# Kernel tuning notes

Measured on AMD Instinct MI355X. Metric: run time of the kernel, lower is better.

The kernel has to match this reference:

```python
import jax, jax.numpy as jnp
import numpy as np

N_NODES = 100000

def _gcn_conv(x, W, b, src, dst, deg_inv_sqrt):
    # h = X W  (dense GEMM)
    h = x @ W
    # symmetric normalization: norm_e = d^{-1/2}[src] * d^{-1/2}[dst]
    norm = deg_inv_sqrt[src] * deg_inv_sqrt[dst]
    # gather-scale-scatter aggregation
    msgs = h[src] * norm[:, None]
    out = jax.ops.segment_sum(msgs, dst, num_segments=N_NODES)
    return out + b

def _prep_graph(edge_index):
    # add self loops (PyG GCNConv default)
    loop = jnp.arange(N_NODES, dtype=edge_index.dtype)
    src = jnp.concatenate([edge_index[0], loop])
    dst = jnp.concatenate([edge_index[1], loop])
    deg = jax.ops.segment_sum(jnp.ones_like(dst, dtype=jnp.float32), dst,
                              num_segments=N_NODES)
    deg_inv_sqrt = jnp.where(deg > 0, jax.lax.rsqrt(deg), 0.0)
    return src, dst, deg_inv_sqrt

def setup_inputs() -> dict:
    key = jax.random.key(0)
    ks = jax.random.split(key, 5)
    d_in, d_h, d_out, E = 128, 256, 128, 1600000
    x = jax.random.normal(ks[0], (N_NODES, d_in), dtype=jnp.float32)
    edge_index = jax.random.randint(ks[1], (2, E), 0, N_NODES, dtype=jnp.int64)
    W1 = jax.random.normal(ks[2], (d_in, d_h), dtype=jnp.float32) / np.sqrt(d_in)
    W2 = jax.random.normal(ks[3], (d_h, d_h), dtype=jnp.float32) / np.sqrt(d_h)
    W3 = jax.random.normal(ks[4], (d_h, d_out), dtype=jnp.float32) / np.sqrt(d_h)
    return {"x": x, "edge_index": edge_index,
            "W1": W1, "b1": jnp.zeros((d_h,), jnp.float32),
            "W2": W2, "b2": jnp.zeros((d_h,), jnp.float32),
            "W3": W3, "b3": jnp.zeros((d_out,), jnp.float32)}

def reference(x, edge_index, W1, b1, W2, b2, W3, b3):
    src, dst, dis = _prep_graph(edge_index)
    h = _gcn_conv(x, W1, b1, src, dst, dis)
    h = jax.nn.relu(h)  # dropout is identity in eval mode
    h = _gcn_conv(h, W2, b2, src, dst, dis)
    h = jax.nn.relu(h)
    out = _gcn_conv(h, W3, b3, src, dst, dis)
    return out
```

## Files before the change

### kernel.cpp

```cpp
#include <hip/hip_runtime.h>
#include <hip/hip_bf16.h>

#define N_NODES 100000
#define M_PAD   100096
#define SCAN_B  98

typedef __attribute__((ext_vector_type(8))) short s8v;
typedef __attribute__((ext_vector_type(4))) float f4v;
typedef unsigned short u16;
typedef unsigned int   u32;

__device__ __forceinline__ u16 f2bf(float v) {
    __hip_bfloat16 b = __float2bfloat16(v);
    return __builtin_bit_cast(u16, b);
}
__device__ __forceinline__ float bf2f(u16 u) {
    u32 t = (u32)u << 16;
    return __builtin_bit_cast(float, t);
}
__device__ __forceinline__ float bflo(u32 p) { return __builtin_bit_cast(float, p << 16); }
__device__ __forceinline__ float bfhi(u32 p) { return __builtin_bit_cast(float, p & 0xffff0000u); }

__device__ __forceinline__ void gl_lds16(const void* g, void* l) {
    __builtin_amdgcn_global_load_lds(
        (const __attribute__((address_space(1))) void*)g,
        (__attribute__((address_space(3))) void*)l, 16, 0, 0);
}


__global__ __launch_bounds__(256) void k_zero_int(int* __restrict__ p, int n) {
    int i = blockIdx.x * 256 + threadIdx.x;
    if (i < n) p[i] = 0;
}

__global__ __launch_bounds__(256) void k_count(const int* __restrict__ ei, int E,
                                               int* __restrict__ cnt) {
    const int h = E >> 1;
    for (int i = blockIdx.x * 256 + threadIdx.x; i < h; i += gridDim.x * 256) {
        const int2 d2 = *reinterpret_cast<const int2*>(ei + E + 2 * i);
        atomicAdd(&cnt[d2.x], 1);
        atomicAdd(&cnt[d2.y], 1);
    }
    if (blockIdx.x == 0 && threadIdx.x == 0 && (E & 1))
        atomicAdd(&cnt[ei[E + E - 1]], 1);
}

__global__ __launch_bounds__(1024) void k_scan_a(const int* __restrict__ cnt,
                                                 int* __restrict__ row_ptr,
                                                 int* __restrict__ bsum,
                                                 float* __restrict__ dis, int n) {
    __shared__ int wsum[16];
    const int tid = threadIdx.x;
    const int lane = tid & 63;
    const int wv = tid >> 6;
    const int i = blockIdx.x * 1024 + tid;
    const int v = (i < n) ? cnt[i] : 0;
    if (i < n) dis[i] = 1.0f / sqrtf((float)(v + 1));
    int x = v;
    #pragma unroll
    for (int d = 1; d < 64; d <<= 1) {
        int t = __shfl_up(x, d, 64);
        if (lane >= d) x += t;
    }
    if (lane == 63) wsum[wv] = x;
    __syncthreads();
    int woff = 0, total = 0;
    #pragma unroll
    for (int w = 0; w < 16; ++w) {
        int s = wsum[w];
        if (w < wv) woff += s;
        total += s;
    }
    if (i < n) row_ptr[i] = woff + x - v;
    if (tid == 0) bsum[blockIdx.x] = total;
}

__global__ __launch_bounds__(128) void k_scan_b(int* __restrict__ bsum,
                                                int* __restrict__ row_ptr,
                                                int nparts, int n, int total_edges) {
    __shared__ int w0tot;
    const int tid = threadIdx.x;
    const int lane = tid & 63;
    const int v = (tid < nparts) ? bsum[tid] : 0;
    int x = v;
    #pragma unroll
    for (int d = 1; d < 64; d <<= 1) {
        int t = __shfl_up(x, d, 64);
        if (lane >= d) x += t;
    }
    if (tid == 63) w0tot = x;
    __syncthreads();
    int excl = x - v + ((tid >= 64) ? w0tot : 0);
    if (tid < nparts) bsum[tid] = excl;
    if (tid == 0) row_ptr[n] = total_edges;
}

__global__ __launch_bounds__(1024) void k_scan_c(int* __restrict__ row_ptr,
                                                 const int* __restrict__ bsum,
                                                 int* __restrict__ cursor, int n) {
    const int i = blockIdx.x * 1024 + threadIdx.x;
    if (i < n) {
        const int r = row_ptr[i] + bsum[blockIdx.x];
        row_ptr[i] = r;
        cursor[i] = r;
    }
}

__global__ __launch_bounds__(256) void k_scatter(const int* __restrict__ ei, int E,
                                                 const float* __restrict__ dis,
                                                 int* __restrict__ cursor,
                                                 int2* __restrict__ edat) {
    const int h = E >> 1;
    for (int i = blockIdx.x * 256 + threadIdx.x; i < h; i += gridDim.x * 256) {
        const int2 s2 = *reinterpret_cast<const int2*>(ei + 2 * i);
        const int2 d2 = *reinterpret_cast<const int2*>(ei + E + 2 * i);
        const int p0 = atomicAdd(&cursor[d2.x], 1);
        edat[p0] = make_int2(s2.x, __float_as_int(dis[s2.x] * dis[d2.x]));
        const int p1 = atomicAdd(&cursor[d2.y], 1);
        edat[p1] = make_int2(s2.y, __float_as_int(dis[s2.y] * dis[d2.y]));
    }
    if (blockIdx.x == 0 && threadIdx.x == 0 && (E & 1)) {
        const int e = E - 1;
        const int s = ei[e], d = ei[E + e];
        const int pos = atomicAdd(&cursor[d], 1);
        edat[pos] = make_int2(s, __float_as_int(dis[s] * dis[d]));
    }
}

__global__ __launch_bounds__(256) void k_prep_w_all(
    const float* __restrict__ W1, const float* __restrict__ W2,
    const float* __restrict__ W3,
    u16* __restrict__ w1h, u16* __restrict__ w1l,
    u16* __restrict__ w2h, u16* __restrict__ w2l,
    u16* __restrict__ w3h, u16* __restrict__ w3l) {
    const int b = blockIdx.x;
    const float* W; u16 *H, *L; int K, N, n;
    if (b < 256)      { W = W1; H = w1h; L = w1l; K = 128; N = 256; n = b; }
    else if (b < 512) { W = W2; H = w2h; L = w2l; K = 256; N = 256; n = b - 256; }
    else              { W = W3; H = w3h; L = w3l; K = 256; N = 128; n = b - 512; }
    for (int k = threadIdx.x; k < K; k += 256) {
        float v = W[(size_t)k * N + n];
        u16 hi = f2bf(v);
        H[(size_t)n * K + k] = hi;
        L[(size_t)n * K + k] = f2bf(v - bf2f(hi));
    }
}

__global__ __launch_bounds__(256) void k_x2bf(const float* __restrict__ x,
                                              u16* __restrict__ xb, long n8) {
    long i = (long)blockIdx.x * 256 + threadIdx.x;
    if (i >= n8) return;
    const float4 a = *reinterpret_cast<const float4*>(x + i * 8);
    const float4 b = *reinterpret_cast<const float4*>(x + i * 8 + 4);
    uint4 p;
    p.x = (u32)f2bf(a.x) | ((u32)f2bf(a.y) << 16);
    p.y = (u32)f2bf(a.z) | ((u32)f2bf(a.w) << 16);
    p.z = (u32)f2bf(b.x) | ((u32)f2bf(b.y) << 16);
    p.w = (u32)f2bf(b.z) | ((u32)f2bf(b.w) << 16);
    *reinterpret_cast<uint4*>(xb + i * 8) = p;
}

template <bool BIAS, bool RELU>
__global__ __launch_bounds__(512, 4) void k_gemm2p(
    const u16* __restrict__ A,
    const u16* __restrict__ Bth, const u16* __restrict__ Btl,
    const float* __restrict__ bias,
    u16* __restrict__ Ch,
    int M, int N, int K) {
    __shared__ u16 As[256 * 32];
    __shared__ u16 Bhs[128 * 32];
    __shared__ u16 Bls[128 * 32];

    const int tid  = threadIdx.x;
    const int wid  = tid >> 6;
    const int lane = tid & 63;
    const int wm = wid >> 1;
    const int wn = wid & 1;
    const int row0 = blockIdx.y * 256;
    const int n0   = blockIdx.x * 128;

    const int srow  = lane >> 2;
    const int sbyte = (lane & 3) * 16;
    const int fr = lane & 15;
    const int kg = (lane >> 4) * 8;

    f4v acc[4][4];
    #pragma unroll
    for (int t = 0; t < 4; ++t)
        #pragma unroll
        for (int u = 0; u < 4; ++u)
            acc[t][u] = (f4v){0.f, 0.f, 0.f, 0.f};

    for (int k0 = 0; k0 < K; k0 += 32) {
        #pragma unroll
        for (int g = 0; g < 2; ++g) {
            const int rloc = wid * 32 + g * 16;
            const size_t ga = (size_t)(row0 + rloc + srow) * K + k0;
            gl_lds16((const char*)(A + ga) + sbyte, &As[rloc * 32]);
        }
        {
            const int rloc = wid * 16;
            const size_t gb = (size_t)(n0 + rloc + srow) * K + k0;
            gl_lds16((const char*)(Bth + gb) + sbyte, &Bhs[rloc * 32]);
            gl_lds16((const char*)(Btl + gb) + sbyte, &Bls[rloc * 32]);
        }
        __syncthreads();

        s8v nh[4], nl[4];
        #pragma unroll
        for (int u = 0; u < 4; ++u) {
            const int rb = (wn * 64 + u * 16 + fr) * 32 + kg;
            nh[u] = *(const s8v*)&Bhs[rb];
            nl[u] = *(const s8v*)&Bls[rb];
        }
        #pragma unroll
        for (int t = 0; t < 4; ++t) {
            const int ra = (wm * 64 + t * 16 + fr) * 32 + kg;
            const s8v m = *(const s8v*)&As[ra];
            #pragma unroll
            for (int u = 0; u < 4; ++u) {
                acc[t][u] = __builtin_amdgcn_mfma_f32_16x16x32_bf16(nh[u], m, acc[t][u], 0, 0, 0);
                acc[t][u] = __builtin_amdgcn_mfma_f32_16x16x32_bf16(nl[u], m, acc[t][u], 0, 0, 0);
            }
        }
        __syncthreads();
    }

    const int ncol = (lane >> 4) * 4;
    #pragma unroll
    for (int t = 0; t < 4; ++t) {
        const int grow = row0 + wm * 64 + t * 16 + fr;
        if (grow < M) {
            #pragma unroll
            for (int u = 0; u < 4; ++u) {
                const int nb = n0 + wn * 64 + u * 16 + ncol;
                float v[4];
                #pragma unroll
                for (int r = 0; r < 4; ++r) {
                    float z = acc[t][u][r];
                    if constexpr (BIAS) z += bias[nb + r];
                    if constexpr (RELU) z = fmaxf(z, 0.f);
                    v[r] = z;
                }
                const size_t off = (size_t)grow * N + nb;
                u16 hi[4];
                #pragma unroll
                for (int r = 0; r < 4; ++r) hi[r] = f2bf(v[r]);
                uint2 ph;
                ph.x = (u32)hi[0] | ((u32)hi[1] << 16);
                ph.y = (u32)hi[2] | ((u32)hi[3] << 16);
                *reinterpret_cast<uint2*>(Ch + off) = ph;
            }
        }
    }
}

template <int D, bool BIAS, bool RELU, int OUT_MODE>
__global__ __launch_bounds__(256) void k_agg(
    const u16* __restrict__ h, const int* __restrict__ row_ptr,
    const int2* __restrict__ edat,
    const float* __restrict__ dis, const float* __restrict__ bias,
    float* __restrict__ outf, u16* __restrict__ outh) {
    constexpr int V = D / 64;
    const int wave = threadIdx.x >> 6;
    const int lane = threadIdx.x & 63;
    const int node = blockIdx.x * 4 + wave;
    if (node >= N_NODES) return;

    const int beg = row_ptr[node];
    const int end = row_ptr[node + 1];
    const int base = lane * V;

    float a[4][V];
    #pragma unroll
    for (int c = 0; c < 4; ++c)
        #pragma unroll
        for (int j = 0; j < V; ++j) a[c][j] = 0.f;

#define LOADV(dst, s) do {                                                    \
        const u16* p_ = h + (size_t)(s) * D + base;                           \
        if constexpr (V == 4) {                                               \
            uint2 t_ = *reinterpret_cast<const uint2*>(p_);                   \
            dst[0] = bflo(t_.x); dst[1] = bfhi(t_.x);                         \
            dst[2] = bflo(t_.y); dst[3] = bfhi(t_.y);                         \
        } else {                                                              \
            u32 t_ = *reinterpret_cast<const u32*>(p_);                       \
            dst[0] = bflo(t_); dst[1] = bfhi(t_);                             \
        }                                                                     \
    } while (0)

    int e = beg;
    for (; e + 8 <= end; e += 8) {
        int2 ed[8];
        float v[8][V];
        #pragma unroll
        for (int j = 0; j < 8; ++j) ed[j] = edat[e + j];
        #pragma unroll
        for (int j = 0; j < 8; ++j) LOADV(v[j], ed[j].x);
        #pragma unroll
        for (int j = 0; j < 8; ++j) {
            const float w = __int_as_float(ed[j].y);
            #pragma unroll
            for (int k = 0; k < V; ++k) a[j & 3][k] += v[j][k] * w;
        }
    }
    for (; e + 2 <= end; e += 2) {
        const int2 e0 = edat[e], e1 = edat[e + 1];
        float v0[V], v1[V];
        LOADV(v0, e0.x); LOADV(v1, e1.x);
        const float w0 = __int_as_float(e0.y), w1 = __int_as_float(e1.y);
        #pragma unroll
        for (int k = 0; k < V; ++k) { a[0][k] += v0[k] * w0; a[1][k] += v1[k] * w1; }
    }
    if (e < end) {
        const int2 e0 = edat[e];
        float v0[V];
        LOADV(v0, e0.x);
        const float w0 = __int_as_float(e0.y);
        #pragma unroll
        for (int k = 0; k < V; ++k) a[2][k] += v0[k] * w0;
    }

    {
        float sw = dis[node];
        sw *= sw;
        float vs[V];
        LOADV(vs, node);
        #pragma unroll
        for (int k = 0; k < V; ++k) a[3][k] += vs[k] * sw;
    }
#undef LOADV

    float r[V];
    #pragma unroll
    for (int j = 0; j < V; ++j) {
        float v = (a[0][j] + a[1][j]) + (a[2][j] + a[3][j]);
        if constexpr (BIAS) v += bias[base + j];
        if constexpr (RELU) v = fmaxf(v, 0.f);
        r[j] = v;
    }

    const size_t off = (size_t)node * D + base;
    if constexpr (OUT_MODE == 1) {
        u16 hi[V];
        #pragma unroll
        for (int j = 0; j < V; ++j) hi[j] = f2bf(r[j]);
        if constexpr (V == 4) {
            uint2 ph;
            ph.x = (u32)hi[0] | ((u32)hi[1] << 16);
            ph.y = (u32)hi[2] | ((u32)hi[3] << 16);
            *reinterpret_cast<uint2*>(outh + off) = ph;
        } else {
            *reinterpret_cast<u32*>(outh + off) = (u32)hi[0] | ((u32)hi[1] << 16);
        }
    } else {
        if constexpr (V == 4) {
            *reinterpret_cast<float4*>(outf + off) = make_float4(r[0], r[1], r[2], r[3]);
        } else {
            *reinterpret_cast<float2*>(outf + off) = make_float2(r[0], r[1]);
        }
    }
}


extern "C" void kernel_launch(void* const* d_in, const int* in_sizes, int n_in,
                              void* d_out, int out_size, void* d_ws, size_t ws_size,
                              hipStream_t stream) {
    const float* x  = (const float*)d_in[0];
    const int*   ei = (const int*)d_in[1];
    const float* W1 = (const float*)d_in[2];
    const float* b1 = (const float*)d_in[3];
    const float* W2 = (const float*)d_in[4];
    const float* b2 = (const float*)d_in[5];
    const float* W3 = (const float*)d_in[6];
    const float* b3 = (const float*)d_in[7];
    float* out = (float*)d_out;

    const int N = N_NODES;
    const int E = in_sizes[1] / 2;

    char* ws = (char*)d_ws;
    size_t o = 0;
    auto take = [&](size_t bytes) {
        void* p = ws + o;
        o += (bytes + 255) & ~(size_t)255;
        return p;
    };
    float* dis     = (float*)take((size_t)N * 4);
    int*   row_ptr = (int*)  take((size_t)(N + 1) * 4);
    int*   cnt_cur = (int*)  take((size_t)N * 4);
    int*   bsum    = (int*)  take((size_t)SCAN_B * 4);
    int2*  edat    = (int2*) take((size_t)E * 8);
    u16* wt1h = (u16*)take((size_t)256 * 128 * 2);
    u16* wt1l = (u16*)take((size_t)256 * 128 * 2);
    u16* wt2h = (u16*)take((size_t)256 * 256 * 2);
    u16* wt2l = (u16*)take((size_t)256 * 256 * 2);
    u16* wt3h = (u16*)take((size_t)128 * 256 * 2);
    u16* wt3l = (u16*)take((size_t)128 * 256 * 2);
    char* slot1 = (char*)take((size_t)M_PAD * 256 * 2);
    char* slot2 = (char*)take((size_t)M_PAD * 256 * 2);
    (void)ws_size; (void)n_in; (void)out_size;

    u16* xb = (u16*)slot1;
    u16* h1 = (u16*)slot1;
    u16* h2 = (u16*)slot1;
    u16* xa = (u16*)slot2;
    u16* g2 = (u16*)slot2;
    u16* g3 = (u16*)slot2;

    const int nb_nodes = (N + 255) / 256;
    const int nb_pairs = ((E / 2) + 255) / 256;

    k_zero_int<<<nb_nodes, 256, 0, stream>>>(cnt_cur, N);
    k_count<<<nb_pairs, 256, 0, stream>>>(ei, E, cnt_cur);
    k_scan_a<<<SCAN_B, 1024, 0, stream>>>(cnt_cur, row_ptr, bsum, dis, N);
    k_scan_b<<<1, 128, 0, stream>>>(bsum, row_ptr, SCAN_B, N, E);
    k_scan_c<<<SCAN_B, 1024, 0, stream>>>(row_ptr, bsum, cnt_cur, N);
    k_scatter<<<nb_pairs, 256, 0, stream>>>(ei, E, dis, cnt_cur, edat);

    k_prep_w_all<<<640, 256, 0, stream>>>(W1, W2, W3, wt1h, wt1l, wt2h, wt2l, wt3h, wt3l);
    const long n8 = (long)N * 128 / 8;
    k_x2bf<<<(int)((n8 + 255) / 256), 256, 0, stream>>>(x, xb, n8);

    const int agg_blocks = (N + 3) / 4;
    const int m_blocks = M_PAD / 256;

    k_agg<128, false, false, 1><<<agg_blocks, 256, 0, stream>>>(
        xb, row_ptr, edat, dis, nullptr, nullptr, xa);
    k_gemm2p<true, true><<<dim3(2, m_blocks), 512, 0, stream>>>(
        xa, wt1h, wt1l, b1, h1, N, 256, 128);

    k_gemm2p<false, false><<<dim3(2, m_blocks), 512, 0, stream>>>(
        h1, wt2h, wt2l, nullptr, g2, N, 256, 256);
    k_agg<256, true, true, 1><<<agg_blocks, 256, 0, stream>>>(
        g2, row_ptr, edat, dis, b2, nullptr, h2);

    k_gemm2p<false, false><<<dim3(1, m_blocks), 512, 0, stream>>>(
        h2, wt3h, wt3l, nullptr, g3, N, 128, 256);
    k_agg<128, true, false, 0><<<agg_blocks, 256, 0, stream>>>(
        g3, row_ptr, edat, dis, b3, out, nullptr);
}
```

Before: 627.3 us.

## Double-buffer GEMM LDS tiles and merge weight/x conversion kernels

The GEMM kernel now uses two LDS buffers and issues the global-to-LDS loads for the next K tile before computing on the current one, with a single barrier per iteration. The aim is to overlap memory latency with MFMA work. This doubles LDS use (48KB per block), which may lower occupancy below the requested 4 blocks per CU. The weight-split and x-to-bf16 conversion kernels are also merged into one launch to save a kernel launch.

```diff
diff --git a/kernel.cpp b/kernel.cpp
--- a/kernel.cpp
+++ b/kernel.cpp
@@ -127,37 +127,37 @@
     }
 }
 
-__global__ __launch_bounds__(256) void k_prep_w_all(
+__global__ __launch_bounds__(256) void k_prep_all(
     const float* __restrict__ W1, const float* __restrict__ W2,
-    const float* __restrict__ W3,
+    const float* __restrict__ W3, const float* __restrict__ x,
     u16* __restrict__ w1h, u16* __restrict__ w1l,
     u16* __restrict__ w2h, u16* __restrict__ w2l,
-    u16* __restrict__ w3h, u16* __restrict__ w3l) {
+    u16* __restrict__ w3h, u16* __restrict__ w3l,
+    u16* __restrict__ xb, long n8) {
     const int b = blockIdx.x;
-    const float* W; u16 *H, *L; int K, N, n;
-    if (b < 256)      { W = W1; H = w1h; L = w1l; K = 128; N = 256; n = b; }
-    else if (b < 512) { W = W2; H = w2h; L = w2l; K = 256; N = 256; n = b - 256; }
-    else              { W = W3; H = w3h; L = w3l; K = 256; N = 128; n = b - 512; }
-    for (int k = threadIdx.x; k < K; k += 256) {
-        float v = W[(size_t)k * N + n];
-        u16 hi = f2bf(v);
-        H[(size_t)n * K + k] = hi;
-        L[(size_t)n * K + k] = f2bf(v - bf2f(hi));
-    }
-}
-
-__global__ __launch_bounds__(256) void k_x2bf(const float* __restrict__ x,
-                                              u16* __restrict__ xb, long n8) {
-    long i = (long)blockIdx.x * 256 + threadIdx.x;
-    if (i >= n8) return;
-    const float4 a = *reinterpret_cast<const float4*>(x + i * 8);
-    const float4 b = *reinterpret_cast<const float4*>(x + i * 8 + 4);
-    uint4 p;
-    p.x = (u32)f2bf(a.x) | ((u32)f2bf(a.y) << 16);
-    p.y = (u32)f2bf(a.z) | ((u32)f2bf(a.w) << 16);
-    p.z = (u32)f2bf(b.x) | ((u32)f2bf(b.y) << 16);
-    p.w = (u32)f2bf(b.z) | ((u32)f2bf(b.w) << 16);
-    *reinterpret_cast<uint4*>(xb + i * 8) = p;
+    if (b < 640) {
+        const float* W; u16 *H, *L; int K, N, n;
+        if (b < 256)      { W = W1; H = w1h; L = w1l; K = 128; N = 256; n = b; }
+        else if (b < 512) { W = W2; H = w2h; L = w2l; K = 256; N = 256; n = b - 256; }
+        else              { W = W3; H = w3h; L = w3l; K = 256; N = 128; n = b - 512; }
+        for (int k = threadIdx.x; k < K; k += 256) {
+            float v = W[(size_t)k * N + n];
+            u16 hi = f2bf(v);
+            H[(size_t)n * K + k] = hi;
+            L[(size_t)n * K + k] = f2bf(v - bf2f(hi));
+        }
+    } else {
+        const long i = (long)(b - 640) * 256 + threadIdx.x;
+        if (i >= n8) return;
+        const float4 a = *reinterpret_cast<const float4*>(x + i * 8);
+        const float4 c = *reinterpret_cast<const float4*>(x + i * 8 + 4);
+        uint4 p;
+        p.x = (u32)f2bf(a.x) | ((u32)f2bf(a.y) << 16);
+        p.y = (u32)f2bf(a.z) | ((u32)f2bf(a.w) << 16);
+        p.z = (u32)f2bf(c.x) | ((u32)f2bf(c.y) << 16);
+        p.w = (u32)f2bf(c.z) | ((u32)f2bf(c.w) << 16);
+        *reinterpret_cast<uint4*>(xb + i * 8) = p;
+    }
 }
 
 template <bool BIAS, bool RELU>
@@ -167,9 +167,9 @@
     const float* __restrict__ bias,
     u16* __restrict__ Ch,
     int M, int N, int K) {
-    __shared__ u16 As[256 * 32];
-    __shared__ u16 Bhs[128 * 32];
-    __shared__ u16 Bls[128 * 32];
+    __shared__ u16 As[2][256 * 32];
+    __shared__ u16 Bhs[2][128 * 32];
+    __shared__ u16 Bls[2][128 * 32];
 
     const int tid  = threadIdx.x;
     const int wid  = tid >> 6;
@@ -184,43 +184,49 @@
     const int fr = lane & 15;
     const int kg = (lane >> 4) * 8;
 
-    f4v acc[4][4];
-    #pragma unroll
-    for (int t = 0; t < 4; ++t)
-        #pragma unroll
-        for (int u = 0; u < 4; ++u)
-            acc[t][u] = (f4v){0.f, 0.f, 0.f, 0.f};
-
-    for (int k0 = 0; k0 < K; k0 += 32) {
+    auto STAGE = [&](int bi, int k0) {
         #pragma unroll
         for (int g = 0; g < 2; ++g) {
             const int rloc = wid * 32 + g * 16;
             const size_t ga = (size_t)(row0 + rloc + srow) * K + k0;
-            gl_lds16((const char*)(A + ga) + sbyte, &As[rloc * 32]);
-        }
-        {
-            const int rloc = wid * 16;
-            const size_t gb = (size_t)(n0 + rloc + srow) * K + k0;
-            gl_lds16((const char*)(Bth + gb) + sbyte, &Bhs[rloc * 32]);
-            gl_lds16((const char*)(Btl + gb) + sbyte, &Bls[rloc * 32]);
-        }
-        __syncthreads();
+            gl_lds16((const char*)(A + ga) + sbyte, &As[bi][rloc * 32]);
+        }
+        const int rloc = wid * 16;
+        const size_t gb = (size_t)(n0 + rloc + srow) * K + k0;
+        gl_lds16((const char*)(Bth + gb) + sbyte, &Bhs[bi][rloc * 32]);
+        gl_lds16((const char*)(Btl + gb) + sbyte, &Bls[bi][rloc * 32]);
+    };
+
+    f4v acc[4][4];
+    #pragma unroll
+    for (int t = 0; t < 4; ++t)
+        #pragma unroll
+        for (int u = 0; u < 4; ++u)
+            acc[t][u] = (f4v){0.f, 0.f, 0.f, 0.f};
+
+    const int nt = K >> 5;
+    STAGE(0, 0);
+    __syncthreads();
+
+    for (int t = 0; t < nt; ++t) {
+        const int cur = t & 1;
+        if (t + 1 < nt) STAGE(cur ^ 1, (t + 1) << 5);
 
         s8v nh[4], nl[4];
         #pragma unroll
         for (int u = 0; u < 4; ++u) {
             const int rb = (wn * 64 + u * 16 + fr) * 32 + kg;
-            nh[u] = *(const s8v*)&Bhs[rb];
-            nl[u] = *(const s8v*)&Bls[rb];
-        }
-        #pragma unroll
-        for (int t = 0; t < 4; ++t) {
-            const int ra = (wm * 64 + t * 16 + fr) * 32 + kg;
-            const s8v m = *(const s8v*)&As[ra];
+            nh[u] = *(const s8v*)&Bhs[cur][rb];
+            nl[u] = *(const s8v*)&Bls[cur][rb];
+        }
+        #pragma unroll
+        for (int tt = 0; tt < 4; ++tt) {
+            const int ra = (wm * 64 + tt * 16 + fr) * 32 + kg;
+            const s8v m = *(const s8v*)&As[cur][ra];
             #pragma unroll
             for (int u = 0; u < 4; ++u) {
-                acc[t][u] = __builtin_amdgcn_mfma_f32_16x16x32_bf16(nh[u], m, acc[t][u], 0, 0, 0);
-                acc[t][u] = __builtin_amdgcn_mfma_f32_16x16x32_bf16(nl[u], m, acc[t][u], 0, 0, 0);
+                acc[tt][u] = __builtin_amdgcn_mfma_f32_16x16x32_bf16(nh[u], m, acc[tt][u], 0, 0, 0);
+                acc[tt][u] = __builtin_amdgcn_mfma_f32_16x16x32_bf16(nl[u], m, acc[tt][u], 0, 0, 0);
             }
         }
         __syncthreads();
@@ -418,9 +424,10 @@
     k_scan_c<<<SCAN_B, 1024, 0, stream>>>(row_ptr, bsum, cnt_cur, N);
     k_scatter<<<nb_pairs, 256, 0, stream>>>(ei, E, dis, cnt_cur, edat);
 
-    k_prep_w_all<<<640, 256, 0, stream>>>(W1, W2, W3, wt1h, wt1l, wt2h, wt2l, wt3h, wt3l);
     const long n8 = (long)N * 128 / 8;
-    k_x2bf<<<(int)((n8 + 255) / 256), 256, 0, stream>>>(x, xb, n8);
+    const int prep_blocks = 640 + (int)((n8 + 255) / 256);
+    k_prep_all<<<prep_blocks, 256, 0, stream>>>(
+        W1, W2, W3, x, wt1h, wt1l, wt2h, wt2l, wt3h, wt3l, xb, n8);
 
     const int agg_blocks = (N + 3) / 4;
     const int m_blocks = M_PAD / 256;
```

Result: no change. 637.1 us (+1.6%).
